# Kernel tuning notes

Hardware: AMD Instinct MI355X
Metric: run time of the kernel (lower is better)

Reference implementation:

```python
import jax, jax.numpy as jnp
import numpy as np

COS_EPS = 1e-8   # torch F.cosine_similarity norm clamp
SIM_EPS = 1e-6   # +1e-6 added to every cosine similarity in get_cossim
LOG_EPS = 1e-6   # +1e-6 inside log in calc_loss


def setup_inputs() -> dict:
    key = jax.random.key(0)
    k1, = jax.random.split(key, 1)
    N, M, D = 1024, 16, 512
    embeddings = jax.random.normal(k1, (N, M, D), dtype=jnp.float32)
    w = jnp.asarray(10.0, dtype=jnp.float32)
    b = jnp.asarray(-5.0, dtype=jnp.float32)
    return {"embeddings": embeddings, "w": w, "b": b}


def _unit(x):
    n = jnp.sqrt(jnp.sum(x * x, axis=-1, keepdims=True))
    return x / jnp.maximum(n, COS_EPS)


def _ge2e_loss(embeddings, w, b):
    N, M, D = embeddings.shape
    e_unit = _unit(embeddings)                              # [N, M, D]

    # full centroids (mean over utterances)
    centroids = jnp.mean(embeddings, axis=1)                # [N, D]
    c_unit = _unit(centroids)                               # [N, D]

    # cosine sim of every utterance vs every speaker centroid
    cossim = jnp.einsum('nmd,kd->nmk', e_unit, c_unit)      # [N, M, N]

    # leave-one-out centroid for own-speaker entries (self-exclusion)
    loo = (jnp.sum(embeddings, axis=1, keepdims=True) - embeddings) / (M - 1)  # [N, M, D]
    diag = jnp.sum(e_unit * _unit(loo), axis=-1)            # [N, M]

    idx = jnp.arange(N)
    cossim = cossim.at[idx, :, idx].set(diag)
    cossim = cossim + SIM_EPS

    sim_matrix = w * cossim + b                             # [N, M, N]

    pos = sim_matrix[idx, :, idx]                           # [N, M]
    neg = jnp.log(jnp.sum(jnp.exp(sim_matrix), axis=2) + LOG_EPS)  # [N, M]
    return jnp.sum(neg - pos)


def reference(embeddings, w, b):
    return _ge2e_loss(embeddings, w, b)
```

## Files before the change

kernel.cpp:

```cpp
#include <hip/hip_runtime.h>

#define N_SPK 1024
#define M_UTT 16
#define D_DIM 512

typedef __attribute__((ext_vector_type(8))) short bf16x8;
typedef __attribute__((ext_vector_type(4))) float f32x4;

__device__ __forceinline__ float wave_sum64(float v) {
  #pragma unroll
  for (int off = 32; off >= 1; off >>= 1) v += __shfl_xor(v, off, 64);
  return v;
}

__device__ __forceinline__ unsigned short f2bf(float x) {
  unsigned int u = __float_as_uint(x);
  unsigned int r = (u + 0x7FFFu + ((u >> 16) & 1u)) >> 16;
  return (unsigned short)r;
}

__device__ __forceinline__ unsigned int pack_bf16(float a, float b) {
  return (unsigned int)f2bf(a) | ((unsigned int)f2bf(b) << 16);
}

__device__ __forceinline__ void gload_lds16(const void* g, void* l) {
  __builtin_amdgcn_global_load_lds(
      (const __attribute__((address_space(1))) void*)g,
      (__attribute__((address_space(3))) void*)l, 16, 0, 0);
}

__global__ __launch_bounds__(256) void prep_kernel(
    const float* __restrict__ emb, const float* __restrict__ wp,
    const float* __restrict__ bp, unsigned int* __restrict__ eU,
    unsigned int* __restrict__ cU, float* __restrict__ pos_out)
{
  const int n = blockIdx.x;
  const int t = threadIdx.x;
  __shared__ float es[M_UTT * D_DIM];
  __shared__ float Sd[D_DIM];
  __shared__ float red[4];
  __shared__ float inv_s[M_UTT];

  const float* base = emb + (size_t)n * (M_UTT * D_DIM);
  #pragma unroll
  for (int i = 0; i < 8; ++i) {
    int s = t + i * 256;
    reinterpret_cast<float4*>(es)[s] = reinterpret_cast<const float4*>(base)[s];
  }
  __syncthreads();

  #pragma unroll
  for (int rep = 0; rep < 2; ++rep) {
    int d = t + rep * 256;
    float s = 0.f;
    #pragma unroll
    for (int m = 0; m < M_UTT; ++m) s += es[m * D_DIM + d];
    Sd[d] = s;
  }
  __syncthreads();

  float p = 0.f;
  #pragma unroll
  for (int rep = 0; rep < 2; ++rep) {
    int d = t + rep * 256;
    float c = Sd[d] * (1.f / M_UTT);
    p += c * c;
  }
  p = wave_sum64(p);
  if ((t & 63) == 0) red[t >> 6] = p;
  __syncthreads();
  float cn2 = red[0] + red[1] + red[2] + red[3];
  float invc = 1.f / fmaxf(sqrtf(cn2), 1e-8f);

  {
    int d = t * 2;
    float c0 = Sd[d] * (1.f / M_UTT) * invc;
    float c1 = Sd[d + 1] * (1.f / M_UTT) * invc;
    cU[n * 256 + t] = pack_bf16(c0, c1);
  }

  const int wid = t >> 6, lane = t & 63;
  const float w = *wp, b = *bp;
  for (int m = wid; m < M_UTT; m += 4) {
    float dot = 0.f, ne = 0.f, nl = 0.f;
    #pragma unroll
    for (int r = 0; r < 8; ++r) {
      int d = lane + r * 64;
      float e = es[m * D_DIM + d];
      float l = Sd[d] - e;
      dot += e * l; ne += e * e; nl += l * l;
    }
    dot = wave_sum64(dot); ne = wave_sum64(ne); nl = wave_sum64(nl);
    if (lane == 0) {
      float inv_e = 1.f / fmaxf(sqrtf(ne), 1e-8f);
      float inv_l = 1.f / fmaxf(sqrtf(nl) * (1.f / (M_UTT - 1)), 1e-8f);
      float diag = dot * (1.f / (M_UTT - 1)) * inv_e * inv_l;
      pos_out[n * M_UTT + m] = w * (diag + 1e-6f) + b;
      inv_s[m] = inv_e;
    }
  }
  __syncthreads();

  #pragma unroll
  for (int i = 0; i < 16; ++i) {
    int p2 = t + i * 256;
    int m = p2 >> 8;
    int d = (p2 & 255) * 2;
    float sc = inv_s[m];
    float x0 = es[m * D_DIM + d] * sc;
    float x1 = es[m * D_DIM + d + 1] * sc;
    eU[(size_t)n * 4096 + p2] = pack_bf16(x0, x1);
  }
}

#define BM 128
#define BN 128
#define BK 64

__global__ __launch_bounds__(256) void mfma_kernel(
    const unsigned short* __restrict__ eU, const unsigned short* __restrict__ cU,
    const float* __restrict__ pos, const float* __restrict__ wp,
    const float* __restrict__ bp, float* __restrict__ partial)
{
  __shared__ unsigned short As[BM * BK];
  __shared__ unsigned short Bs[BN * BK];
  __shared__ float rowsum[2][BM];
  __shared__ float pos_l[BM];

  const int t = threadIdx.x;
  const int lane = t & 63;
  const int wv_id = t >> 6;
  const int wm = wv_id >> 1, wn = wv_id & 1;
  const int cb = blockIdx.x, rb = blockIdx.y;
  const int row0 = rb * BM, col0 = cb * BN;

  if (t < BM) pos_l[t] = pos[row0 + t];

  const float w = *wp, b = *bp;
  const float bb = w * 1e-6f + b;

  f32x4 acc[4][4] = {};

  const int lrow = lane >> 3;
  const int lseg = (lane & 7) ^ lrow;

  for (int kt = 0; kt < D_DIM / BK; ++kt) {
    const int d0 = kt * BK;
    __syncthreads();
    #pragma unroll
    for (int i = 0; i < 4; ++i) {
      int c = wv_id * 4 + i;
      size_t gr = (size_t)(row0 + c * 8 + lrow) * D_DIM + d0 + lseg * 8;
      gload_lds16(eU + gr, (char*)As + c * 1024);
      size_t gc = (size_t)(col0 + c * 8 + lrow) * D_DIM + d0 + lseg * 8;
      gload_lds16(cU + gc, (char*)Bs + c * 1024);
    }
    __syncthreads();

    #pragma unroll
    for (int kk = 0; kk < 2; ++kk) {
      bf16x8 af[4], bf[4];
      #pragma unroll
      for (int mi = 0; mi < 4; ++mi) {
        int r = wm * 64 + mi * 16 + (lane & 15);
        int seg = ((lane >> 4) + kk * 4) ^ (r & 7);
        af[mi] = *reinterpret_cast<const bf16x8*>(
            (const char*)As + r * 128 + seg * 16);
      }
      #pragma unroll
      for (int nj = 0; nj < 4; ++nj) {
        int s = wn * 64 + nj * 16 + (lane & 15);
        int seg = ((lane >> 4) + kk * 4) ^ (s & 7);
        bf[nj] = *reinterpret_cast<const bf16x8*>(
            (const char*)Bs + s * 128 + seg * 16);
      }
      #pragma unroll
      for (int mi = 0; mi < 4; ++mi)
        #pragma unroll
        for (int nj = 0; nj < 4; ++nj)
          acc[mi][nj] = __builtin_amdgcn_mfma_f32_16x16x32_bf16(
              af[mi], bf[nj], acc[mi][nj], 0, 0, 0);
    }
  }

  float esum[4][4];
  #pragma unroll
  for (int mi = 0; mi < 4; ++mi)
    #pragma unroll
    for (int rg = 0; rg < 4; ++rg) esum[mi][rg] = 0.f;

  #pragma unroll
  for (int nj = 0; nj < 4; ++nj) {
    int kg = col0 + wn * 64 + nj * 16 + (lane & 15);
    #pragma unroll
    for (int mi = 0; mi < 4; ++mi) {
      #pragma unroll
      for (int rg = 0; rg < 4; ++rg) {
        int r_loc = wm * 64 + mi * 16 + (lane >> 4) * 4 + rg;
        float arg = w * acc[mi][nj][rg] + bb;
        if (kg == ((row0 + r_loc) >> 4)) arg = pos_l[r_loc];
        esum[mi][rg] += __expf(arg);
      }
    }
  }
  #pragma unroll
  for (int mi = 0; mi < 4; ++mi)
    #pragma unroll
    for (int rg = 0; rg < 4; ++rg) {
      float v = esum[mi][rg];
      v += __shfl_xor(v, 1, 64);
      v += __shfl_xor(v, 2, 64);
      v += __shfl_xor(v, 4, 64);
      v += __shfl_xor(v, 8, 64);
      esum[mi][rg] = v;
    }
  if ((lane & 15) == 0) {
    #pragma unroll
    for (int mi = 0; mi < 4; ++mi)
      #pragma unroll
      for (int rg = 0; rg < 4; ++rg)
        rowsum[wn][wm * 64 + mi * 16 + (lane >> 4) * 4 + rg] = esum[mi][rg];
  }
  __syncthreads();
  if (t < BM) partial[(size_t)cb * (N_SPK * M_UTT) + row0 + t] =
      rowsum[0][t] + rowsum[1][t];
}

__global__ __launch_bounds__(256) void finalize_kernel(
    const float* __restrict__ partial, const float* __restrict__ pos,
    float* __restrict__ bsum)
{
  const int t = threadIdx.x;
  const int r = blockIdx.x * 256 + t;
  float s = 0.f;
  #pragma unroll
  for (int cb = 0; cb < 8; ++cb) s += partial[cb * (N_SPK * M_UTT) + r];
  float v = logf(s + 1e-6f) - pos[r];
  v = wave_sum64(v);
  __shared__ float red[4];
  if ((t & 63) == 0) red[t >> 6] = v;
  __syncthreads();
  if (t == 0) bsum[blockIdx.x] = red[0] + red[1] + red[2] + red[3];
}

__global__ void final_reduce(const float* __restrict__ bsum,
                             float* __restrict__ out)
{
  float v = bsum[threadIdx.x];
  v = wave_sum64(v);
  if (threadIdx.x == 0) out[0] = v;
}

extern "C" void kernel_launch(void* const* d_in, const int* in_sizes, int n_in,
                              void* d_out, int out_size, void* d_ws, size_t ws_size,
                              hipStream_t stream) {
  const float* emb = (const float*)d_in[0];
  const float* wp  = (const float*)d_in[1];
  const float* bp  = (const float*)d_in[2];
  float* out = (float*)d_out;

  char* wsb = (char*)d_ws;
  unsigned int* eU  = (unsigned int*)wsb;
  unsigned int* cU  = (unsigned int*)(wsb + 16777216);
  float* pos        = (float*)(wsb + 16777216 + 1048576);
  float* partial    = (float*)(wsb + 16777216 + 1048576 + 65536);
  float* bsum       = (float*)(wsb + 16777216 + 1048576 + 65536 + 524288);

  prep_kernel<<<N_SPK, 256, 0, stream>>>(emb, wp, bp, eU, cU, pos);
  dim3 grid(N_SPK / BN, (N_SPK * M_UTT) / BM);
  mfma_kernel<<<grid, 256, 0, stream>>>(
      (const unsigned short*)eU, (const unsigned short*)cU, pos, wp, bp, partial);
  finalize_kernel<<<(N_SPK * M_UTT) / 256, 256, 0, stream>>>(partial, pos, bsum);
  final_reduce<<<1, 64, 0, stream>>>(bsum, out);
}
```

Baseline: 51.51 us.

## Restructure similarity GEMM into 256x256 tiles with a four-stage async LDS pipeline

The MFMA kernel now uses 256x256 output tiles with 512 threads, so each of the 8 waves computes a 128x64 sub-tile. The K dimension is staged 32 elements at a time through a four-deep LDS ring buffer filled by global_load_lds, with explicit vmcnt waits and barriers so loads overlap compute. It also remaps block IDs (swizzle) and raises wave priority around the MFMA bursts. The aim is better operand reuse and hidden global-load latency, but the grid shrinks to 256 blocks. That removes spare parallelism, and the large LDS footprint limits occupancy to one block per CU.

```diff
diff --git a/kernel.cpp b/kernel.cpp
--- a/kernel.cpp
+++ b/kernel.cpp
@@ -113,90 +113,124 @@
   }
 }
 
-#define BM 128
-#define BN 128
-#define BK 64
-
-__global__ __launch_bounds__(256) void mfma_kernel(
-    const unsigned short* __restrict__ eU, const unsigned short* __restrict__ cU,
+#define NTILES 16
+
+struct StageOff { unsigned int gA0, gA1, gB0, gB1; int c0off, c1off; };
+
+__device__ __forceinline__ void stage_tile(
+    const char* __restrict__ eU, const char* __restrict__ cU,
+    char* AsB, int t, const StageOff& so)
+{
+  const int buf = t & 3;
+  const int d0b = t * 64;
+  char* Ab = AsB + buf * 16384;
+  char* Bb = AsB + 65536 + buf * 16384;
+  gload_lds16(eU + so.gA0 + d0b, Ab + so.c0off);
+  gload_lds16(eU + so.gA1 + d0b, Ab + so.c1off);
+  gload_lds16(cU + so.gB0 + d0b, Bb + so.c0off);
+  gload_lds16(cU + so.gB1 + d0b, Bb + so.c1off);
+}
+
+__device__ __forceinline__ void compute_tile(
+    const char* AsB, int t, int wm, int wn, int laneoff, f32x4 acc[8][4])
+{
+  const int buf = t & 3;
+  const char* Ab = AsB + buf * 16384;
+  const char* Bb = AsB + 65536 + buf * 16384;
+  bf16x8 af[8], bfr[4];
+  #pragma unroll
+  for (int mi = 0; mi < 8; ++mi)
+    af[mi] = *reinterpret_cast<const bf16x8*>(Ab + (wm * 128 + mi * 16) * 64 + laneoff);
+  #pragma unroll
+  for (int nj = 0; nj < 4; ++nj)
+    bfr[nj] = *reinterpret_cast<const bf16x8*>(Bb + (wn * 64 + nj * 16) * 64 + laneoff);
+  __builtin_amdgcn_s_setprio(1);
+  #pragma unroll
+  for (int mi = 0; mi < 8; ++mi)
+    #pragma unroll
+    for (int nj = 0; nj < 4; ++nj)
+      acc[mi][nj] = __builtin_amdgcn_mfma_f32_16x16x32_bf16(
+          af[mi], bfr[nj], acc[mi][nj], 0, 0, 0);
+  __builtin_amdgcn_s_setprio(0);
+}
+
+__global__ __launch_bounds__(512, 2) void mfma_kernel(
+    const char* __restrict__ eU, const char* __restrict__ cU,
     const float* __restrict__ pos, const float* __restrict__ wp,
     const float* __restrict__ bp, float* __restrict__ partial)
 {
-  __shared__ unsigned short As[BM * BK];
-  __shared__ unsigned short Bs[BN * BK];
-  __shared__ float rowsum[2][BM];
-  __shared__ float pos_l[BM];
+  __shared__ char AsB[131072];
+  __shared__ float pos_l[256];
+  __shared__ float rowsum[4][256];
 
   const int t = threadIdx.x;
   const int lane = t & 63;
-  const int wv_id = t >> 6;
-  const int wm = wv_id >> 1, wn = wv_id & 1;
-  const int cb = blockIdx.x, rb = blockIdx.y;
-  const int row0 = rb * BM, col0 = cb * BN;
-
-  if (t < BM) pos_l[t] = pos[row0 + t];
+  const int wv = t >> 6;
+  const int wm = wv >> 2, wn = wv & 3;
+
+  const int bid = blockIdx.x;
+  const int sw = (bid & 7) * 32 + (bid >> 3);
+  const int cb = sw & 3, rb = sw >> 2;
+  const int row0 = rb * 256, col0 = cb * 256;
 
   const float w = *wp, b = *bp;
   const float bb = w * 1e-6f + b;
 
-  f32x4 acc[4][4] = {};
-
-  const int lrow = lane >> 3;
-  const int lseg = (lane & 7) ^ lrow;
-
-  for (int kt = 0; kt < D_DIM / BK; ++kt) {
-    const int d0 = kt * BK;
-    __syncthreads();
-    #pragma unroll
-    for (int i = 0; i < 4; ++i) {
-      int c = wv_id * 4 + i;
-      size_t gr = (size_t)(row0 + c * 8 + lrow) * D_DIM + d0 + lseg * 8;
-      gload_lds16(eU + gr, (char*)As + c * 1024);
-      size_t gc = (size_t)(col0 + c * 8 + lrow) * D_DIM + d0 + lseg * 8;
-      gload_lds16(cU + gc, (char*)Bs + c * 1024);
-    }
-    __syncthreads();
-
-    #pragma unroll
-    for (int kk = 0; kk < 2; ++kk) {
-      bf16x8 af[4], bf[4];
-      #pragma unroll
-      for (int mi = 0; mi < 4; ++mi) {
-        int r = wm * 64 + mi * 16 + (lane & 15);
-        int seg = ((lane >> 4) + kk * 4) ^ (r & 7);
-        af[mi] = *reinterpret_cast<const bf16x8*>(
-            (const char*)As + r * 128 + seg * 16);
-      }
-      #pragma unroll
-      for (int nj = 0; nj < 4; ++nj) {
-        int s = wn * 64 + nj * 16 + (lane & 15);
-        int seg = ((lane >> 4) + kk * 4) ^ (s & 7);
-        bf[nj] = *reinterpret_cast<const bf16x8*>(
-            (const char*)Bs + s * 128 + seg * 16);
-      }
-      #pragma unroll
-      for (int mi = 0; mi < 4; ++mi)
-        #pragma unroll
-        for (int nj = 0; nj < 4; ++nj)
-          acc[mi][nj] = __builtin_amdgcn_mfma_f32_16x16x32_bf16(
-              af[mi], bf[nj], acc[mi][nj], 0, 0, 0);
-    }
-  }
-
-  float esum[4][4];
-  #pragma unroll
-  for (int mi = 0; mi < 4; ++mi)
+  if (t < 256) pos_l[t] = pos[row0 + t];
+
+  StageOff so;
+  {
+    const int seg = (lane & 7) ^ (lane >> 3);
+    const int p = seg >> 2, ks = seg & 3;
+    const int rA0 = ((2 * wv) * 8 + (lane >> 3)) * 2 + p;
+    const int rA1 = ((2 * wv + 1) * 8 + (lane >> 3)) * 2 + p;
+    so.gA0 = (unsigned int)(row0 + rA0) * 1024u + ks * 16;
+    so.gA1 = (unsigned int)(row0 + rA1) * 1024u + ks * 16;
+    so.gB0 = (unsigned int)(col0 + rA0) * 1024u + ks * 16;
+    so.gB1 = (unsigned int)(col0 + rA1) * 1024u + ks * 16;
+    so.c0off = (2 * wv) * 1024;
+    so.c1off = (2 * wv + 1) * 1024;
+  }
+  const int j = lane & 15, g = lane >> 4;
+  const int laneoff = (j >> 1) * 128 + ((((j & 1) * 4 + g) ^ (j >> 1)) * 16);
+
+  f32x4 acc[8][4] = {};
+
+  __syncthreads();
+
+  stage_tile(eU, cU, AsB, 0, so);
+  stage_tile(eU, cU, AsB, 1, so);
+  stage_tile(eU, cU, AsB, 2, so);
+
+  for (int tt = 0; tt < NTILES - 2; ++tt) {
+    asm volatile("s_waitcnt vmcnt(8)" ::: "memory");
+    __builtin_amdgcn_s_barrier();
+    if (tt < NTILES - 3) stage_tile(eU, cU, AsB, tt + 3, so);
+    compute_tile(AsB, tt, wm, wn, laneoff, acc);
+    __builtin_amdgcn_s_barrier();
+  }
+  asm volatile("s_waitcnt vmcnt(4)" ::: "memory");
+  __builtin_amdgcn_s_barrier();
+  compute_tile(AsB, NTILES - 2, wm, wn, laneoff, acc);
+  __builtin_amdgcn_s_barrier();
+  asm volatile("s_waitcnt vmcnt(0)" ::: "memory");
+  __builtin_amdgcn_s_barrier();
+  compute_tile(AsB, NTILES - 1, wm, wn, laneoff, acc);
+
+  float esum[8][4];
+  #pragma unroll
+  for (int mi = 0; mi < 8; ++mi)
     #pragma unroll
     for (int rg = 0; rg < 4; ++rg) esum[mi][rg] = 0.f;
 
   #pragma unroll
   for (int nj = 0; nj < 4; ++nj) {
-    int kg = col0 + wn * 64 + nj * 16 + (lane & 15);
-    #pragma unroll
-    for (int mi = 0; mi < 4; ++mi) {
+    const int kg = col0 + wn * 64 + nj * 16 + (lane & 15);
+    #pragma unroll
+    for (int mi = 0; mi < 8; ++mi) {
       #pragma unroll
       for (int rg = 0; rg < 4; ++rg) {
-        int r_loc = wm * 64 + mi * 16 + (lane >> 4) * 4 + rg;
+        const int r_loc = wm * 128 + mi * 16 + (lane >> 4) * 4 + rg;
         float arg = w * acc[mi][nj][rg] + bb;
         if (kg == ((row0 + r_loc) >> 4)) arg = pos_l[r_loc];
         esum[mi][rg] += __expf(arg);
@@ -204,7 +238,7 @@
     }
   }
   #pragma unroll
-  for (int mi = 0; mi < 4; ++mi)
+  for (int mi = 0; mi < 8; ++mi)
     #pragma unroll
     for (int rg = 0; rg < 4; ++rg) {
       float v = esum[mi][rg];
@@ -216,14 +250,15 @@
     }
   if ((lane & 15) == 0) {
     #pragma unroll
-    for (int mi = 0; mi < 4; ++mi)
+    for (int mi = 0; mi < 8; ++mi)
       #pragma unroll
       for (int rg = 0; rg < 4; ++rg)
-        rowsum[wn][wm * 64 + mi * 16 + (lane >> 4) * 4 + rg] = esum[mi][rg];
-  }
-  __syncthreads();
-  if (t < BM) partial[(size_t)cb * (N_SPK * M_UTT) + row0 + t] =
-      rowsum[0][t] + rowsum[1][t];
+        rowsum[wn][wm * 128 + mi * 16 + (lane >> 4) * 4 + rg] = esum[mi][rg];
+  }
+  __syncthreads();
+  if (t < 256)
+    partial[(size_t)cb * (N_SPK * M_UTT) + row0 + t] =
+        rowsum[0][t] + rowsum[1][t] + rowsum[2][t] + rowsum[3][t];
 }
 
 __global__ __launch_bounds__(256) void finalize_kernel(
@@ -234,7 +269,7 @@
   const int r = blockIdx.x * 256 + t;
   float s = 0.f;
   #pragma unroll
-  for (int cb = 0; cb < 8; ++cb) s += partial[cb * (N_SPK * M_UTT) + r];
+  for (int cb = 0; cb < 4; ++cb) s += partial[cb * (N_SPK * M_UTT) + r];
   float v = logf(s + 1e-6f) - pos[r];
   v = wave_sum64(v);
   __shared__ float red[4];
@@ -264,12 +299,11 @@
   unsigned int* cU  = (unsigned int*)(wsb + 16777216);
   float* pos        = (float*)(wsb + 16777216 + 1048576);
   float* partial    = (float*)(wsb + 16777216 + 1048576 + 65536);
-  float* bsum       = (float*)(wsb + 16777216 + 1048576 + 65536 + 524288);
+  float* bsum       = (float*)(wsb + 16777216 + 1048576 + 65536 + 262144);
 
   prep_kernel<<<N_SPK, 256, 0, stream>>>(emb, wp, bp, eU, cU, pos);
-  dim3 grid(N_SPK / BN, (N_SPK * M_UTT) / BM);
-  mfma_kernel<<<grid, 256, 0, stream>>>(
-      (const unsigned short*)eU, (const unsigned short*)cU, pos, wp, bp, partial);
+  mfma_kernel<<<256, 512, 0, stream>>>(
+      (const char*)eU, (const char*)cU, pos, wp, bp, partial);
   finalize_kernel<<<(N_SPK * M_UTT) / 256, 256, 0, stream>>>(partial, pos, bsum);
   final_reduce<<<1, 64, 0, stream>>>(bsum, out);
 }
```

Result: faster. 45.67 us (-11.3%).
